# Optimization experiments

Measured on AMD Instinct MI355X. Metric: run time of the kernel, lower is better.

The kernel has to match this reference:

```python
import jax, jax.numpy as jnp
import numpy as np

# 3x3 laplacian stencil, OIHW
LAP = jnp.array([-1, -1, -1, -1, 8, -1, -1, -1, -1], dtype=jnp.float32).reshape(1, 1, 3, 3)
THR = 0.1
SMOOTH = 1.0


def _lap_conv(x, stride):
    # x: [B,1,H,W]
    return jax.lax.conv_general_dilated(
        x, LAP, window_strides=(stride, stride), padding=((1, 1), (1, 1)),
        dimension_numbers=('NCHW', 'OIHW', 'NCHW'))


def _nearest_up(x, H, W):
    # PyTorch 'nearest': src_idx = floor(dst_idx * in/out)
    h, w = x.shape[2], x.shape[3]
    ri = (jnp.arange(H) * h) // H
    ci = (jnp.arange(W) * w) // W
    return x[:, :, ri][:, :, :, ci]


def _thresh(x):
    return jnp.where(x > THR, 1.0, 0.0).astype(x.dtype)


def setup_inputs() -> dict:
    key = jax.random.key(0)
    k1, k2 = jax.random.split(key)
    B, H, W = 16, 1024, 1024
    boundary_logits = jax.random.normal(k1, (B, 1, H, W), dtype=jnp.float32)
    gtmasks = (jax.random.uniform(k2, (B, H, W)) > 0.5).astype(jnp.float32)
    fuse_kernel = jnp.array([0.6, 0.3, 0.1], dtype=jnp.float32).reshape(1, 3, 1, 1)
    return {"boundary_logits": boundary_logits, "gtmasks": gtmasks, "fuse_kernel": fuse_kernel}


def reference(boundary_logits, gtmasks, fuse_kernel):
    g = gtmasks[:, None, :, :].astype(jnp.float32)  # [B,1,H,W]
    bt = _thresh(jnp.maximum(_lap_conv(g, 1), 0.0))  # full res
    H, W = bt.shape[2], bt.shape[3]
    bt2 = _thresh(_nearest_up(jnp.maximum(_lap_conv(g, 2), 0.0), H, W))
    bt4 = _thresh(_nearest_up(jnp.maximum(_lap_conv(g, 4), 0.0), H, W))
    # (x8 branch in original is computed but unused in the output)
    pyr = jnp.concatenate([bt, bt2, bt4], axis=1)  # [B,3,H,W]
    fused = jnp.einsum('bchw,c->bhw', pyr, fuse_kernel.reshape(3))[:, None]  # 1x1 fuse conv
    target = _thresh(fused)  # [B,1,H,W]

    x = boundary_logits
    # stable BCE with logits, mean reduction
    bce_loss = jnp.mean(jnp.maximum(x, 0.0) - x * target + jnp.log1p(jnp.exp(-jnp.abs(x))))

    p = jax.nn.sigmoid(x)
    n = p.shape[0]
    pf = p.reshape(n, -1)
    tf = target.reshape(n, -1)
    inter = jnp.sum(pf * tf, axis=1)
    dice_loss = jnp.mean(1.0 - (2.0 * inter + SMOOTH) / (jnp.sum(pf, 1) + jnp.sum(tf, 1) + SMOOTH))
    return bce_loss, dice_loss
```

## Files before the change

kernel.cpp:

```cpp
#include <hip/hip_runtime.h>

#define IMG_H 1024
#define IMG_W 1024
#define NIMG  16
#define NPIX  16777216.0f
#define SPI   128
#define NBLK  2048
#define LOG2E 1.44269504088896340736f
#define LN2   0.69314718055994530942f


__global__ __launch_bounds__(256) void dal_main(
    const float* __restrict__ xlogits,
    const float* __restrict__ gmask,
    const float* __restrict__ fuse,
    float4* __restrict__ ws4)
{
    const int bid  = blockIdx.x;
    const int img  = bid >> 7;
    const int q    = bid & 127;
    const int r0   = q << 3;
    const int tid  = (int)threadIdx.x;
    const int lane = tid & 63;
    const int j0   = tid * 4;

    const float w0 = fuse[0], w1 = fuse[1], w2 = fuse[2];

    const size_t ibase = (size_t)img * (IMG_H * IMG_W);
    const float* gi = gmask + ibase;
    const float* xi = xlogits + ibase;

    const int  jl   = (j0 > 0) ? (j0 - 1) : 0;
    const int  jr1  = (j0 + 4 < IMG_W) ? (j0 + 1) : (IMG_W - 4);
    const bool hasL = (j0 > 0);
    const bool hasR = (j0 + 4 < IMG_W);

    float rm[10][4];
    float cv[8][4];
    #pragma unroll
    for (int t = 0; t < 10; ++t) {
        const int r = r0 - 1 + t;
        float c0 = 0.f, c1 = 0.f, c2 = 0.f, c3 = 0.f, c4 = 0.f, c5 = 0.f;
        if (r >= 0 && r < IMG_H) {
            const float* row = gi + (size_t)r * IMG_W;
            float4 a = *reinterpret_cast<const float4*>(row + jl);
            float4 b = *reinterpret_cast<const float4*>(row + jr1);
            c0 = hasL ? a.x : 0.f;
            c1 = hasL ? a.y : a.x;
            c2 = hasL ? a.z : a.y;
            c3 = hasL ? a.w : a.z;
            c4 = hasR ? b.z : b.w;
            c5 = hasR ? b.w : 0.f;
        }
        rm[t][0] = fminf(c0, fminf(c1, c2));
        rm[t][1] = fminf(c1, fminf(c2, c3));
        rm[t][2] = fminf(c2, fminf(c3, c4));
        rm[t][3] = fminf(c3, fminf(c4, c5));
        if (t >= 1 && t <= 8) {
            cv[t - 1][0] = c1; cv[t - 1][1] = c2;
            cv[t - 1][2] = c3; cv[t - 1][3] = c4;
        }
    }

    float bt[8][4];
    #pragma unroll
    for (int r = 0; r < 8; ++r)
        #pragma unroll
        for (int k = 0; k < 4; ++k) {
            float cm = fminf(rm[r][k], fminf(rm[r + 1][k], rm[r + 2][k]));
            bt[r][k] = (cv[r][k] > 0.5f && cm < 0.5f) ? 1.f : 0.f;
        }

    const float wb4A = w2 * bt[0][0];
    const float wb4B = w2 * bt[4][0];
    float base2[4][2];
    #pragma unroll
    for (int rp = 0; rp < 4; ++rp) {
        const float wb = (rp < 2) ? wb4A : wb4B;
        base2[rp][0] = fmaf(w1, bt[2 * rp][0], wb);
        base2[rp][1] = fmaf(w1, bt[2 * rp][2], wb);
    }

    float l2[2]  = {0.f, 0.f}, xt[2] = {0.f, 0.f};
    float itr[2] = {0.f, 0.f}, sp[2] = {0.f, 0.f};
    int st = 0;

    auto px = [&](float x, float btv, float b2v, int a) {
        float f = fmaf(w0, btv, b2v);
        bool  c = f > 0.1f;
        st += (int)__popcll(__ballot(c));
        float u   = __builtin_amdgcn_exp2f(x * LOG2E);
        float opu = 1.f + u;
        float p   = u * __builtin_amdgcn_rcpf(opu);
        l2[a]  += __builtin_amdgcn_logf(opu);
        sp[a]  += p;
        xt[a]  += c ? x : 0.f;
        itr[a] += c ? p : 0.f;
    };

    const float* xrow = xi + (size_t)r0 * IMG_W + j0;
    #pragma unroll
    for (int r = 0; r < 8; ++r) {
        float4 xv = *reinterpret_cast<const float4*>(xrow + (size_t)r * IMG_W);
        const int   rp = r >> 1;
        const int   a  = r & 1;
        const float bA = base2[rp][0];
        const float bB = base2[rp][1];
        px(xv.x, bt[r][0], bA, a);
        px(xv.y, bt[r][1], bA, a);
        px(xv.z, bt[r][2], bB, a);
        px(xv.w, bt[r][3], bB, a);
    }

    float bce   = fmaf(LN2, l2[0] + l2[1], -(xt[0] + xt[1]));
    float inter = itr[0] + itr[1];
    float sump  = sp[0] + sp[1];

    #pragma unroll
    for (int off = 32; off > 0; off >>= 1) {
        bce   += __shfl_down(bce, off);
        inter += __shfl_down(inter, off);
        sump  += __shfl_down(sump, off);
    }
    __shared__ float red[4][4];
    const int wid = tid >> 6;
    if (lane == 0) {
        red[0][wid] = bce; red[1][wid] = inter;
        red[2][wid] = sump; red[3][wid] = (float)st;
    }
    __syncthreads();
    if (tid == 0) {
        float4 o;
        o.x = red[0][0] + red[0][1] + red[0][2] + red[0][3];
        o.y = red[1][0] + red[1][1] + red[1][2] + red[1][3];
        o.z = red[2][0] + red[2][1] + red[2][2] + red[2][3];
        o.w = red[3][0] + red[3][1] + red[3][2] + red[3][3];
        ws4[bid] = o;
    }
}

__global__ __launch_bounds__(1024) void dal_finalize(
    const float4* __restrict__ ws4, float* __restrict__ out)
{
    const int t    = (int)threadIdx.x;
    const int wv   = t >> 6;
    const int lane = t & 63;

    float4 a = ws4[2 * t];
    float4 b = ws4[2 * t + 1];
    float bce   = a.x + b.x;
    float inter = a.y + b.y;
    float sump  = a.z + b.z;
    float sumt  = a.w + b.w;

    #pragma unroll
    for (int off = 32; off > 0; off >>= 1) {
        bce   += __shfl_down(bce, off);
        inter += __shfl_down(inter, off);
        sump  += __shfl_down(sump, off);
        sumt  += __shfl_down(sumt, off);
    }

    __shared__ float sb[16], sd[16];
    if (lane == 0) {
        sb[wv] = bce;
        sd[wv] = 1.f - (2.f * inter + 1.f) / (sump + sumt + 1.f);
    }
    __syncthreads();
    if (t == 0) {
        float tb = 0.f, td = 0.f;
        #pragma unroll
        for (int i = 0; i < NIMG; ++i) { tb += sb[i]; td += sd[i]; }
        out[0] = tb / NPIX;
        out[1] = td / (float)NIMG;
    }
}

extern "C" void kernel_launch(void* const* d_in, const int* in_sizes, int n_in,
                              void* d_out, int out_size, void* d_ws, size_t ws_size,
                              hipStream_t stream)
{
    const float* x    = (const float*)d_in[0];
    const float* g    = (const float*)d_in[1];
    const float* fuse = (const float*)d_in[2];
    float* out = (float*)d_out;
    float4* ws4 = (float4*)d_ws;

    dal_main<<<NBLK, 256, 0, stream>>>(x, g, fuse, ws4);
    dal_finalize<<<1, 1024, 0, stream>>>(ws4, out);
}
```

Before: 31.12 us.

## Stage mask rows in LDS via async global_load_lds and stream stencil rows

Mask rows (10 per block) are copied into shared memory with the direct global-to-LDS load builtin instead of two overlapping float4 register loads per row. Neighbour pixels are then read from LDS, and the logit loads are issued before the barrier so they overlap the staging. The 3x3 min stencil is restructured into a rolling two-row window to cut register pressure, with launch bounds raised to request more occupancy. The cost is 40KB of LDS per block, which may itself limit occupancy, plus an extra barrier.

Result: slower. 32.09 us (+3.1%).

```diff
diff --git a/kernel.cpp b/kernel.cpp
--- a/kernel.cpp
+++ b/kernel.cpp
@@ -4,23 +4,40 @@
 #define IMG_W 1024
 #define NIMG  16
 #define NPIX  16777216.0f
-#define SPI   128
 #define NBLK  2048
 #define LOG2E 1.44269504088896340736f
 #define LN2   0.69314718055994530942f
 
-
-__global__ __launch_bounds__(256) void dal_main(
+#ifndef __has_builtin
+#define __has_builtin(x) 0
+#endif
+
+__device__ __forceinline__ void stage16(const float* src, float* dstLds, int lane) {
+#if __has_builtin(__builtin_amdgcn_global_load_lds)
+    __builtin_amdgcn_global_load_lds(
+        (const __attribute__((address_space(1))) void*)src,
+        (__attribute__((address_space(3))) void*)dstLds,
+        16, 0, 0);
+#else
+    *reinterpret_cast<float4*>(dstLds + (lane << 2)) =
+        *reinterpret_cast<const float4*>(src);
+#endif
+}
+
+
+__global__ __launch_bounds__(256, 4) void dal_main(
     const float* __restrict__ xlogits,
     const float* __restrict__ gmask,
     const float* __restrict__ fuse,
     float4* __restrict__ ws4)
 {
-    const int bid  = blockIdx.x;
-    const int img  = bid >> 7;
-    const int q    = bid & 127;
-    const int r0   = q << 3;
+    __shared__ float lds[10 * 1024];
+
+    const int b    = blockIdx.x;
+    const int img  = b >> 7;
+    const int r0   = (b & 127) << 3;
     const int tid  = (int)threadIdx.x;
+    const int wid  = tid >> 6;
     const int lane = tid & 63;
     const int j0   = tid * 4;
 
@@ -30,56 +47,39 @@
     const float* gi = gmask + ibase;
     const float* xi = xlogits + ibase;
 
-    const int  jl   = (j0 > 0) ? (j0 - 1) : 0;
-    const int  jr1  = (j0 + 4 < IMG_W) ? (j0 + 1) : (IMG_W - 4);
+    #pragma unroll
+    for (int t = 0; t < 10; ++t) {
+        int r  = r0 - 1 + t;
+        int rc = r < 0 ? 0 : (r > IMG_H - 1 ? IMG_H - 1 : r);
+        stage16(gi + (size_t)rc * IMG_W + j0, &lds[t * 1024 + (wid << 8)], lane);
+    }
+
+    float4 xv[8];
+    const float* xr = xi + (size_t)r0 * IMG_W + j0;
+    #pragma unroll
+    for (int r = 0; r < 8; ++r)
+        xv[r] = *reinterpret_cast<const float4*>(xr + (size_t)r * IMG_W);
+
+    __syncthreads();
+
     const bool hasL = (j0 > 0);
     const bool hasR = (j0 + 4 < IMG_W);
-
-    float rm[10][4];
-    float cv[8][4];
-    #pragma unroll
-    for (int t = 0; t < 10; ++t) {
-        const int r = r0 - 1 + t;
-        float c0 = 0.f, c1 = 0.f, c2 = 0.f, c3 = 0.f, c4 = 0.f, c5 = 0.f;
-        if (r >= 0 && r < IMG_H) {
-            const float* row = gi + (size_t)r * IMG_W;
-            float4 a = *reinterpret_cast<const float4*>(row + jl);
-            float4 b = *reinterpret_cast<const float4*>(row + jr1);
-            c0 = hasL ? a.x : 0.f;
-            c1 = hasL ? a.y : a.x;
-            c2 = hasL ? a.z : a.y;
-            c3 = hasL ? a.w : a.z;
-            c4 = hasR ? b.z : b.w;
-            c5 = hasR ? b.w : 0.f;
-        }
-        rm[t][0] = fminf(c0, fminf(c1, c2));
-        rm[t][1] = fminf(c1, fminf(c2, c3));
-        rm[t][2] = fminf(c2, fminf(c3, c4));
-        rm[t][3] = fminf(c3, fminf(c4, c5));
-        if (t >= 1 && t <= 8) {
-            cv[t - 1][0] = c1; cv[t - 1][1] = c2;
-            cv[t - 1][2] = c3; cv[t - 1][3] = c4;
-        }
-    }
-
-    float bt[8][4];
-    #pragma unroll
-    for (int r = 0; r < 8; ++r)
-        #pragma unroll
-        for (int k = 0; k < 4; ++k) {
-            float cm = fminf(rm[r][k], fminf(rm[r + 1][k], rm[r + 2][k]));
-            bt[r][k] = (cv[r][k] > 0.5f && cm < 0.5f) ? 1.f : 0.f;
-        }
-
-    const float wb4A = w2 * bt[0][0];
-    const float wb4B = w2 * bt[4][0];
-    float base2[4][2];
-    #pragma unroll
-    for (int rp = 0; rp < 4; ++rp) {
-        const float wb = (rp < 2) ? wb4A : wb4B;
-        base2[rp][0] = fmaf(w1, bt[2 * rp][0], wb);
-        base2[rp][1] = fmaf(w1, bt[2 * rp][2], wb);
-    }
+    const int  jl   = hasL ? j0 - 1 : 0;
+    const int  jr   = hasR ? j0 + 4 : IMG_W - 1;
+
+    auto fold = [&](int t, float* rm, float* cvo) {
+        const float* Lr = &lds[t * 1024];
+        float4 v   = *reinterpret_cast<const float4*>(Lr + j0);
+        float  lf0 = Lr[jl];
+        float  rg0 = Lr[jr];
+        float  lf  = hasL ? lf0 : 0.f;
+        float  rg  = hasR ? rg0 : 0.f;
+        rm[0] = fminf(lf,  fminf(v.x, v.y));
+        rm[1] = fminf(v.x, fminf(v.y, v.z));
+        rm[2] = fminf(v.y, fminf(v.z, v.w));
+        rm[3] = fminf(v.z, fminf(v.w, rg));
+        cvo[0] = v.x; cvo[1] = v.y; cvo[2] = v.z; cvo[3] = v.w;
+    };
 
     float l2[2]  = {0.f, 0.f}, xt[2] = {0.f, 0.f};
     float itr[2] = {0.f, 0.f}, sp[2] = {0.f, 0.f};
@@ -98,18 +98,47 @@
         itr[a] += c ? p : 0.f;
     };
 
-    const float* xrow = xi + (size_t)r0 * IMG_W + j0;
-    #pragma unroll
-    for (int r = 0; r < 8; ++r) {
-        float4 xv = *reinterpret_cast<const float4*>(xrow + (size_t)r * IMG_W);
-        const int   rp = r >> 1;
-        const int   a  = r & 1;
-        const float bA = base2[rp][0];
-        const float bB = base2[rp][1];
-        px(xv.x, bt[r][0], bA, a);
-        px(xv.y, bt[r][1], bA, a);
-        px(xv.z, bt[r][2], bB, a);
-        px(xv.w, bt[r][3], bB, a);
+    float rm0[4], rm1[4], rm2[4], rm3[4], cvA[4], cvB[4], cvC[4], tmp[4];
+    fold(0, rm0, tmp);
+    if (r0 == 0) { rm0[0] = rm0[1] = rm0[2] = rm0[3] = 0.f; }
+    fold(1, rm1, cvA);
+    float wb4A = 0.f, wb4B = 0.f;
+
+    #pragma unroll
+    for (int rp = 0; rp < 4; ++rp) {
+        fold(2 * rp + 2, rm2, cvB);
+        fold(2 * rp + 3, rm3, cvC);
+        if (rp == 3 && r0 == IMG_H - 8) {
+            rm3[0] = rm3[1] = rm3[2] = rm3[3] = 0.f;
+        }
+
+        float bta[4], btb[4];
+        #pragma unroll
+        for (int k = 0; k < 4; ++k) {
+            float cma = fminf(rm0[k], fminf(rm1[k], rm2[k]));
+            float cmb = fminf(rm1[k], fminf(rm2[k], rm3[k]));
+            bta[k] = (cvA[k] > 0.5f && cma < 0.5f) ? 1.f : 0.f;
+            btb[k] = (cvB[k] > 0.5f && cmb < 0.5f) ? 1.f : 0.f;
+        }
+        if (rp == 0) wb4A = w2 * bta[0];
+        if (rp == 2) wb4B = w2 * bta[0];
+        const float wb  = (rp < 2) ? wb4A : wb4B;
+        const float b20 = fmaf(w1, bta[0], wb);
+        const float b21 = fmaf(w1, bta[2], wb);
+
+        px(xv[2 * rp].x,     bta[0], b20, 0);
+        px(xv[2 * rp].y,     bta[1], b20, 0);
+        px(xv[2 * rp].z,     bta[2], b21, 0);
+        px(xv[2 * rp].w,     bta[3], b21, 0);
+        px(xv[2 * rp + 1].x, btb[0], b20, 1);
+        px(xv[2 * rp + 1].y, btb[1], b20, 1);
+        px(xv[2 * rp + 1].z, btb[2], b21, 1);
+        px(xv[2 * rp + 1].w, btb[3], b21, 1);
+
+        #pragma unroll
+        for (int k = 0; k < 4; ++k) {
+            rm0[k] = rm2[k]; rm1[k] = rm3[k]; cvA[k] = cvC[k];
+        }
     }
 
     float bce   = fmaf(LN2, l2[0] + l2[1], -(xt[0] + xt[1]));
@@ -122,20 +151,21 @@
         inter += __shfl_down(inter, off);
         sump  += __shfl_down(sump, off);
     }
-    __shared__ float red[4][4];
-    const int wid = tid >> 6;
+    __syncthreads();
     if (lane == 0) {
-        red[0][wid] = bce; red[1][wid] = inter;
-        red[2][wid] = sump; red[3][wid] = (float)st;
+        lds[wid]      = bce;
+        lds[4 + wid]  = inter;
+        lds[8 + wid]  = sump;
+        lds[12 + wid] = (float)st;
     }
     __syncthreads();
     if (tid == 0) {
         float4 o;
-        o.x = red[0][0] + red[0][1] + red[0][2] + red[0][3];
-        o.y = red[1][0] + red[1][1] + red[1][2] + red[1][3];
-        o.z = red[2][0] + red[2][1] + red[2][2] + red[2][3];
-        o.w = red[3][0] + red[3][1] + red[3][2] + red[3][3];
-        ws4[bid] = o;
+        o.x = (lds[0]  + lds[1])  + (lds[2]  + lds[3]);
+        o.y = (lds[4]  + lds[5])  + (lds[6]  + lds[7]);
+        o.z = (lds[8]  + lds[9])  + (lds[10] + lds[11]);
+        o.w = (lds[12] + lds[13]) + (lds[14] + lds[15]);
+        ws4[b] = o;
     }
 }
 
@@ -147,11 +177,11 @@
     const int lane = t & 63;
 
     float4 a = ws4[2 * t];
-    float4 b = ws4[2 * t + 1];
-    float bce   = a.x + b.x;
-    float inter = a.y + b.y;
-    float sump  = a.z + b.z;
-    float sumt  = a.w + b.w;
+    float4 bq = ws4[2 * t + 1];
+    float bce   = a.x + bq.x;
+    float inter = a.y + bq.y;
+    float sump  = a.z + bq.z;
+    float sumt  = a.w + bq.w;
 
     #pragma unroll
     for (int off = 32; off > 0; off >>= 1) {
```
